# Optimization experiments

Measured on AMD Instinct MI355X. Metric: run time of the kernel, lower is better.

The kernel has to match this reference:

```python
import jax, jax.numpy as jnp
import numpy as np

N_NODES = 100000
N_EDGES = 3200000
DIM = 128
HID = 32


def gcn_conv(x, src, dst, W, b, n):
    # PyG GCNConv: linear transform, add self-loops, symmetric deg normalization,
    # scatter-sum to destination, then bias.
    x = x @ W  # [N, out]
    loops = jnp.arange(n)
    s = jnp.concatenate([src, loops])
    d = jnp.concatenate([dst, loops])
    deg = jax.ops.segment_sum(jnp.ones(s.shape[0], x.dtype), d, num_segments=n)
    dinv = jax.lax.rsqrt(deg)  # deg >= 1 thanks to self-loops
    norm = dinv[s] * dinv[d]   # [E+N]
    out = jax.ops.segment_sum(x[s] * norm[:, None], d, num_segments=n)
    return out + b


def setup_inputs() -> dict:
    key = jax.random.key(0)
    k = jax.random.split(key, 4)
    x = jax.random.normal(k[0], (N_NODES, DIM), dtype=jnp.float32)
    edge_index = jax.random.randint(k[1], (2, N_EDGES), 0, N_NODES)
    W1 = jax.random.normal(k[2], (DIM, HID), dtype=jnp.float32) * (1.0 / np.sqrt(DIM))
    b1 = jnp.zeros((HID,), jnp.float32)
    W2 = jax.random.normal(k[3], (HID, 1), dtype=jnp.float32) * (1.0 / np.sqrt(HID))
    b2 = jnp.zeros((1,), jnp.float32)
    return {"x": x, "edge_index": edge_index, "W1": W1, "b1": b1, "W2": W2, "b2": b2}


def reference(x, edge_index, W1, b1, W2, b2):
    src, dst = edge_index[0], edge_index[1]
    n = x.shape[0]
    h = jax.nn.relu(gcn_conv(x, src, dst, W1, b1, n))        # [N, 32]
    scores = gcn_conv(h, src, dst, W2, b2, n).squeeze(-1)     # [N]
    return (h, scores)
```

## Files before the change

### kernel.cpp

```cpp
#include <hip/hip_runtime.h>
#include <hip/hip_bf16.h>

#define N_NODES 100000
#define N_EDGES 3200000
#define DIM 128
#define HID 32

#define BSH 6
#define BNODES (1 << BSH)
#define NBUK ((N_NODES + BNODES - 1) >> BSH)
#define NBP 2048
#define FCHUNK 8192
#define NFILL ((N_EDGES + FCHUNK - 1) / FCHUNK)
#define CAP 3072

typedef short v8s __attribute__((ext_vector_type(8)));
typedef float v4f __attribute__((ext_vector_type(4)));

__device__ __forceinline__ float bf_lo(unsigned int u) { return __uint_as_float(u << 16); }
__device__ __forceinline__ float bf_hi(unsigned int u) { return __uint_as_float(u & 0xFFFF0000u); }
__device__ __forceinline__ unsigned int pk2(float a, float b) {
    __hip_bfloat162 p = __float22bfloat162_rn(make_float2(a, b));
    union { __hip_bfloat162 h; unsigned int u; } cv; cv.h = p; return cv.u;
}


__global__ void k_zeroB(int* __restrict__ bcnt) {
    int i = blockIdx.x * blockDim.x + threadIdx.x;
    if (i < NBP) bcnt[i] = 0;
}

__launch_bounds__(512)
__global__ void k_bfill(const int* __restrict__ src, const int* __restrict__ dst,
                        int* __restrict__ bcnt, unsigned int* __restrict__ ebuf) {
    __shared__ int cntA[NBP];
    __shared__ int offA[NBP];
    __shared__ int baseG[NBP];
    __shared__ int ssum[512];
    __shared__ unsigned int stage[FCHUNK];
    __shared__ unsigned short sbuk[FCHUNK];
    int t = threadIdx.x;
    int e0 = blockIdx.x * FCHUNK;
    int eN = min(e0 + FCHUNK, N_EDGES) - e0;
    int n4 = eN >> 2;
    const int4* d4 = (const int4*)(dst + e0);
    const int4* s4 = (const int4*)(src + e0);
    int4 dd[4], ss[4];
    #pragma unroll
    for (int k = 0; k < 4; ++k) {
        int i = t + k * 512;
        if (i < n4) { dd[k] = d4[i]; ss[k] = s4[i]; }
    }
    for (int i = t; i < NBP; i += 512) cntA[i] = 0;
    __syncthreads();
    unsigned short rk[16];
    #pragma unroll
    for (int k = 0; k < 4; ++k) {
        int i = t + k * 512;
        if (i < n4) {
            rk[4 * k + 0] = (unsigned short)atomicAdd(&cntA[dd[k].x >> BSH], 1);
            rk[4 * k + 1] = (unsigned short)atomicAdd(&cntA[dd[k].y >> BSH], 1);
            rk[4 * k + 2] = (unsigned short)atomicAdd(&cntA[dd[k].z >> BSH], 1);
            rk[4 * k + 3] = (unsigned short)atomicAdd(&cntA[dd[k].w >> BSH], 1);
        }
    }
    __syncthreads();
    {
        int c[4]; int sum = 0;
        #pragma unroll
        for (int k = 0; k < 4; ++k) { c[k] = cntA[t * 4 + k]; sum += c[k]; }
        ssum[t] = sum; __syncthreads();
        for (int d = 1; d < 512; d <<= 1) {
            int add = (t >= d) ? ssum[t - d] : 0;
            __syncthreads();
            ssum[t] += add;
            __syncthreads();
        }
        int excl = ssum[t] - sum;
        #pragma unroll
        for (int k = 0; k < 4; ++k) { offA[t * 4 + k] = excl; excl += c[k]; }
    }
    __syncthreads();
    for (int b = t; b < NBP; b += 512)
        if (cntA[b] > 0) baseG[b] = b * CAP + atomicAdd(&bcnt[b], cntA[b]);
    #pragma unroll
    for (int k = 0; k < 4; ++k) {
        int i = t + k * 512;
        if (i < n4) {
            int b0 = dd[k].x >> BSH, b1 = dd[k].y >> BSH;
            int b2 = dd[k].z >> BSH, b3 = dd[k].w >> BSH;
            int p0 = offA[b0] + rk[4 * k + 0];
            int p1 = offA[b1] + rk[4 * k + 1];
            int p2 = offA[b2] + rk[4 * k + 2];
            int p3 = offA[b3] + rk[4 * k + 3];
            stage[p0] = ((unsigned int)(dd[k].x & (BNODES - 1)) << 20) | (unsigned int)ss[k].x;
            stage[p1] = ((unsigned int)(dd[k].y & (BNODES - 1)) << 20) | (unsigned int)ss[k].y;
            stage[p2] = ((unsigned int)(dd[k].z & (BNODES - 1)) << 20) | (unsigned int)ss[k].z;
            stage[p3] = ((unsigned int)(dd[k].w & (BNODES - 1)) << 20) | (unsigned int)ss[k].w;
            sbuk[p0] = (unsigned short)b0;
            sbuk[p1] = (unsigned short)b1;
            sbuk[p2] = (unsigned short)b2;
            sbuk[p3] = (unsigned short)b3;
        }
    }
    __syncthreads();
    for (int i = t; i < eN; i += 512) {
        int b = sbuk[i];
        ebuf[baseG[b] + (i - offA[b])] = stage[i];
    }
}

__launch_bounds__(256)
__global__ void k_sort(unsigned int* __restrict__ ebuf, const int* __restrict__ bcnt,
                       int* __restrict__ rowbeg, int* __restrict__ rowend,
                       float* __restrict__ dinv) {
    __shared__ unsigned int slab[CAP];
    __shared__ unsigned int slab2[CAP];
    __shared__ int hist[BNODES];
    __shared__ int scanx[BNODES];
    __shared__ int cur[BNODES];
    int t = threadIdx.x;
    int b = blockIdx.x;
    int s0 = b * CAP;
    int n = min(bcnt[b], CAP);
    if (t < BNODES) hist[t] = 0;
    __syncthreads();
    for (int i = t; i < n; i += 256) {
        unsigned int w = ebuf[s0 + i];
        slab[i] = w;
        atomicAdd(&hist[w >> 20], 1);
    }
    __syncthreads();
    if (t == 0) {
        int r = 0;
        for (int l = 0; l < BNODES; ++l) { scanx[l] = r; r += hist[l]; }
    }
    __syncthreads();
    if (t < BNODES) {
        cur[t] = scanx[t];
        int v = b * BNODES + t;
        if (v < N_NODES) {
            rowbeg[v] = s0 + scanx[t];
            rowend[v] = s0 + scanx[t] + hist[t];
            dinv[v] = rsqrtf((float)(hist[t] + 1));
        }
    }
    __syncthreads();
    for (int i = t; i < n; i += 256) {
        unsigned int w = slab[i];
        int pos = atomicAdd(&cur[w >> 20], 1);
        slab2[pos] = w;
    }
    __syncthreads();
    for (int i = t; i < n; i += 256) ebuf[s0 + i] = slab2[i];
}

__launch_bounds__(256)
__global__ void k_gemm1(const float* __restrict__ x, const float* __restrict__ W1,
                        const float* __restrict__ dinv, unsigned int* __restrict__ y1a,
                        unsigned int* __restrict__ y1b) {
    int wv = (blockIdx.x * 256 + threadIdx.x) >> 6;
    int nwaves = (gridDim.x * 256) >> 6;
    int lane = threadIdx.x & 63;
    int m = lane & 15;
    int kb = lane >> 4;
    v8s Bf[2][4];
    #pragma unroll
    for (int tt = 0; tt < 2; ++tt)
        #pragma unroll
        for (int s = 0; s < 4; ++s) {
            union { unsigned int u[4]; v8s v; } ub;
            #pragma unroll
            for (int jj = 0; jj < 4; ++jj) {
                int k = s * 32 + kb * 8 + jj * 2;
                ub.u[jj] = pk2(W1[k * HID + tt * 16 + m], W1[(k + 1) * HID + tt * 16 + m]);
            }
            Bf[tt][s] = ub.v;
        }
    for (int tile = wv; tile < N_NODES / 16; tile += nwaves) {
        int base = tile * 16;
        const float* xr = x + (size_t)(base + m) * DIM;
        v4f acc0 = {0.f, 0.f, 0.f, 0.f}, acc1 = {0.f, 0.f, 0.f, 0.f};
        #pragma unroll
        for (int s = 0; s < 4; ++s) {
            float4 xa = *(const float4*)(xr + s * 32 + kb * 8);
            float4 xb = *(const float4*)(xr + s * 32 + kb * 8 + 4);
            union { unsigned int u[4]; v8s v; } ua;
            ua.u[0] = pk2(xa.x, xa.y); ua.u[1] = pk2(xa.z, xa.w);
            ua.u[2] = pk2(xb.x, xb.y); ua.u[3] = pk2(xb.z, xb.w);
            acc0 = __builtin_amdgcn_mfma_f32_16x16x32_bf16(ua.v, Bf[0][s], acc0, 0, 0, 0);
            acc1 = __builtin_amdgcn_mfma_f32_16x16x32_bf16(ua.v, Bf[1][s], acc1, 0, 0, 0);
        }
        float4 dv = *(const float4*)(dinv + base + kb * 4);
        float d[4] = {dv.x, dv.y, dv.z, dv.w};
        #pragma unroll
        for (int r = 0; r < 4; ++r) {
            float v0 = acc0[r] * d[r];
            float v1 = acc1[r] * d[r];
            float p0 = __shfl_xor(v0, 1, 64);
            float p1 = __shfl_xor(v1, 1, 64);
            if ((m & 1) == 0) {
                int node = base + kb * 4 + r;
                y1a[node * 8 + (m >> 1)] = pk2(v0, p0);
                y1b[node * 8 + (m >> 1)] = pk2(v1, p1);
            }
        }
    }
}

template <int HALF>
__launch_bounds__(256)
__global__ void k_gather1(const int* __restrict__ rowbeg, const int* __restrict__ rowend,
                          const unsigned int* __restrict__ ebuf,
                          const unsigned int* __restrict__ yh, const float* __restrict__ dinv,
                          const float* __restrict__ b1, const float* __restrict__ W2,
                          float* __restrict__ out_h, float* __restrict__ pA,
                          float* __restrict__ y2) {
    int t = threadIdx.x;
    int node = blockIdx.x * 8 + (t >> 5);
    if (node >= N_NODES) return;
    int lane = t & 31;
    int sub = lane >> 2;
    int c2 = lane & 3;
    int start = rowbeg[node], end = rowend[node];
    float a0[4] = {0.f, 0.f, 0.f, 0.f};
    float a1[4] = {0.f, 0.f, 0.f, 0.f};
    float a2[4] = {0.f, 0.f, 0.f, 0.f};
    float a3[4] = {0.f, 0.f, 0.f, 0.f};
    const uint2* y2b = (const uint2*)yh;
    int j = start;
    for (; j + 32 <= end; j += 32) {
        unsigned int w = ebuf[j + lane];
        unsigned int e0 = (unsigned int)__shfl((int)w, 0  + sub, 32) & 0xFFFFF;
        unsigned int e1 = (unsigned int)__shfl((int)w, 8  + sub, 32) & 0xFFFFF;
        unsigned int e2 = (unsigned int)__shfl((int)w, 16 + sub, 32) & 0xFFFFF;
        unsigned int e3 = (unsigned int)__shfl((int)w, 24 + sub, 32) & 0xFFFFF;
        uint2 v0 = y2b[e0 * 4 + c2];
        uint2 v1 = y2b[e1 * 4 + c2];
        uint2 v2 = y2b[e2 * 4 + c2];
        uint2 v3 = y2b[e3 * 4 + c2];
        a0[0] += bf_lo(v0.x); a0[1] += bf_hi(v0.x); a0[2] += bf_lo(v0.y); a0[3] += bf_hi(v0.y);
        a1[0] += bf_lo(v1.x); a1[1] += bf_hi(v1.x); a1[2] += bf_lo(v1.y); a1[3] += bf_hi(v1.y);
        a2[0] += bf_lo(v2.x); a2[1] += bf_hi(v2.x); a2[2] += bf_lo(v2.y); a2[3] += bf_hi(v2.y);
        a3[0] += bf_lo(v3.x); a3[1] += bf_hi(v3.x); a3[2] += bf_lo(v3.y); a3[3] += bf_hi(v3.y);
    }
    int navail = end - j;
    if (navail > 0) {
        unsigned int w = ebuf[min(j + lane, end - 1)];
        #pragma unroll
        for (int k = 0; k < 4; ++k) {
            int idx = k * 8 + sub;
            unsigned int u = (unsigned int)__shfl((int)w, idx, 32) & 0xFFFFF;
            if (idx < navail) {
                uint2 v = y2b[u * 4 + c2];
                a0[0] += bf_lo(v.x); a0[1] += bf_hi(v.x);
                a0[2] += bf_lo(v.y); a0[3] += bf_hi(v.y);
            }
        }
    }
    float q[4];
    #pragma unroll
    for (int i = 0; i < 4; ++i) q[i] = (a0[i] + a1[i]) + (a2[i] + a3[i]);
    #pragma unroll
    for (int i = 0; i < 4; ++i) {
        q[i] += __shfl_xor(q[i], 4, 32);
        q[i] += __shfl_xor(q[i], 8, 32);
        q[i] += __shfl_xor(q[i], 16, 32);
    }
    uint2 sv = y2b[(unsigned int)node * 4 + c2];
    q[0] += bf_lo(sv.x); q[1] += bf_hi(sv.x); q[2] += bf_lo(sv.y); q[3] += bf_hi(sv.y);
    float di = dinv[node];
    int col = HALF * 16 + 4 * c2;
    float h[4], p = 0.f;
    #pragma unroll
    for (int i = 0; i < 4; ++i) {
        h[i] = fmaxf(fmaf(di, q[i], b1[col + i]), 0.f);
        p = fmaf(h[i], W2[col + i], p);
    }
    p += __shfl_xor(p, 1, 32);
    p += __shfl_xor(p, 2, 32);
    if (sub == 0) {
        *(float4*)&out_h[(size_t)node * HID + col] = make_float4(h[0], h[1], h[2], h[3]);
        if (c2 == 0) {
            if (HALF == 0) pA[node] = p;
            else           y2[node] = di * (pA[node] + p);
        }
    }
}

__launch_bounds__(256)
__global__ void k_gather2(const int* __restrict__ rowbeg, const int* __restrict__ rowend,
                          const unsigned int* __restrict__ ebuf, const float* __restrict__ y2,
                          const float* __restrict__ dinv, const float* __restrict__ b2,
                          float* __restrict__ scores) {
    int t = threadIdx.x;
    int node = blockIdx.x * 8 + (t >> 5);
    int lane = t & 31;
    if (node >= N_NODES) return;
    int start = rowbeg[node], end = rowend[node];
    float acc = 0.f;
    for (int j = start + lane; j < end; j += 32)
        acc += y2[ebuf[j] & 0xFFFFF];
    #pragma unroll
    for (int off = 16; off > 0; off >>= 1) acc += __shfl_xor(acc, off);
    if (lane == 0) scores[node] = dinv[node] * (acc + y2[node]) + b2[0];
}

extern "C" void kernel_launch(void* const* d_in, const int* in_sizes, int n_in,
                              void* d_out, int out_size, void* d_ws, size_t ws_size,
                              hipStream_t stream) {
    const float* x  = (const float*)d_in[0];
    const int* ei   = (const int*)d_in[1];
    const float* W1 = (const float*)d_in[2];
    const float* b1 = (const float*)d_in[3];
    const float* W2 = (const float*)d_in[4];
    const float* b2 = (const float*)d_in[5];

    const int* src = ei;
    const int* dst = ei + N_EDGES;

    int* bcnt = (int*)d_ws;
    unsigned int* ebuf = (unsigned int*)(bcnt + NBP);
    int* rowbeg = (int*)(ebuf + (size_t)NBUK * CAP);
    int* rowend = rowbeg + N_NODES;
    float* dinv = (float*)(rowend + N_NODES);
    unsigned int* y1a = (unsigned int*)(dinv + N_NODES);
    unsigned int* y1b = y1a + (size_t)N_NODES * 8;
    float* pA   = (float*)(y1b + (size_t)N_NODES * 8);
    float* y2   = pA + N_NODES;

    float* out_h = (float*)d_out;
    float* out_s = out_h + (size_t)N_NODES * HID;

    k_zeroB <<<NBP / 256, 256, 0, stream>>>(bcnt);
    k_bfill <<<NFILL, 512, 0, stream>>>(src, dst, bcnt, ebuf);
    k_sort  <<<NBUK, 256, 0, stream>>>(ebuf, bcnt, rowbeg, rowend, dinv);
    k_gemm1 <<<512, 256, 0, stream>>>(x, W1, dinv, y1a, y1b);
    k_gather1<0><<<(N_NODES + 7) / 8, 256, 0, stream>>>(rowbeg, rowend, ebuf, y1a, dinv, b1, W2, out_h, pA, y2);
    k_gather1<1><<<(N_NODES + 7) / 8, 256, 0, stream>>>(rowbeg, rowend, ebuf, y1b, dinv, b1, W2, out_h, pA, y2);
    k_gather2<<<(N_NODES + 7) / 8, 256, 0, stream>>>(rowbeg, rowend, ebuf, y2, dinv, b2, out_s);
}
```

Baseline: 137.1 us.

## Shrink fill chunk, fold bucket offsets, and split sort histogram into sub-counters

Reduces the edge-fill chunk per block from 8192 to 6144 edges, which lowers shared memory per block and raises the block count. It replaces the separate global-base and offset lookups with one precomputed difference array per bucket. In the per-bucket sort kernel, the 64-entry histogram and cursor arrays become four sub-counters per node chosen by thread index, which spreads LDS atomic contention. The cost is extra scan work and more fill blocks issuing global atomics.

After: 146.3 us. 6.7% more time.

```diff
diff --git a/kernel.cpp b/kernel.cpp
--- a/kernel.cpp
+++ b/kernel.cpp
@@ -10,7 +10,7 @@
 #define BNODES (1 << BSH)
 #define NBUK ((N_NODES + BNODES - 1) >> BSH)
 #define NBP 2048
-#define FCHUNK 8192
+#define FCHUNK 6144
 #define NFILL ((N_EDGES + FCHUNK - 1) / FCHUNK)
 #define CAP 3072
 
@@ -35,7 +35,7 @@
                         int* __restrict__ bcnt, unsigned int* __restrict__ ebuf) {
     __shared__ int cntA[NBP];
     __shared__ int offA[NBP];
-    __shared__ int baseG[NBP];
+    __shared__ int diff[NBP];
     __shared__ int ssum[512];
     __shared__ unsigned int stage[FCHUNK];
     __shared__ unsigned short sbuk[FCHUNK];
@@ -45,17 +45,17 @@
     int n4 = eN >> 2;
     const int4* d4 = (const int4*)(dst + e0);
     const int4* s4 = (const int4*)(src + e0);
-    int4 dd[4], ss[4];
-    #pragma unroll
-    for (int k = 0; k < 4; ++k) {
+    int4 dd[3], ss[3];
+    #pragma unroll
+    for (int k = 0; k < 3; ++k) {
         int i = t + k * 512;
         if (i < n4) { dd[k] = d4[i]; ss[k] = s4[i]; }
     }
     for (int i = t; i < NBP; i += 512) cntA[i] = 0;
     __syncthreads();
-    unsigned short rk[16];
-    #pragma unroll
-    for (int k = 0; k < 4; ++k) {
+    unsigned short rk[12];
+    #pragma unroll
+    for (int k = 0; k < 3; ++k) {
         int i = t + k * 512;
         if (i < n4) {
             rk[4 * k + 0] = (unsigned short)atomicAdd(&cntA[dd[k].x >> BSH], 1);
@@ -82,9 +82,9 @@
     }
     __syncthreads();
     for (int b = t; b < NBP; b += 512)
-        if (cntA[b] > 0) baseG[b] = b * CAP + atomicAdd(&bcnt[b], cntA[b]);
-    #pragma unroll
-    for (int k = 0; k < 4; ++k) {
+        if (cntA[b] > 0) diff[b] = b * CAP + atomicAdd(&bcnt[b], cntA[b]) - offA[b];
+    #pragma unroll
+    for (int k = 0; k < 3; ++k) {
         int i = t + k * 512;
         if (i < n4) {
             int b0 = dd[k].x >> BSH, b1 = dd[k].y >> BSH;
@@ -104,10 +104,8 @@
         }
     }
     __syncthreads();
-    for (int i = t; i < eN; i += 512) {
-        int b = sbuk[i];
-        ebuf[baseG[b] + (i - offA[b])] = stage[i];
-    }
+    for (int i = t; i < eN; i += 512)
+        ebuf[diff[sbuk[i]] + i] = stage[i];
 }
 
 __launch_bounds__(256)
@@ -116,39 +114,50 @@
                        float* __restrict__ dinv) {
     __shared__ unsigned int slab[CAP];
     __shared__ unsigned int slab2[CAP];
-    __shared__ int hist[BNODES];
+    __shared__ int hist4[BNODES * 4];
     __shared__ int scanx[BNODES];
-    __shared__ int cur[BNODES];
+    __shared__ int cur4[BNODES * 4];
     int t = threadIdx.x;
     int b = blockIdx.x;
     int s0 = b * CAP;
     int n = min(bcnt[b], CAP);
-    if (t < BNODES) hist[t] = 0;
-    __syncthreads();
+    if (t < BNODES * 4) hist4[t] = 0;
+    __syncthreads();
+    int sub = t & 3;
     for (int i = t; i < n; i += 256) {
         unsigned int w = ebuf[s0 + i];
         slab[i] = w;
-        atomicAdd(&hist[w >> 20], 1);
+        atomicAdd(&hist4[((w >> 20) << 2) + sub], 1);
     }
     __syncthreads();
     if (t == 0) {
         int r = 0;
-        for (int l = 0; l < BNODES; ++l) { scanx[l] = r; r += hist[l]; }
+        for (int l = 0; l < BNODES; ++l) {
+            scanx[l] = r;
+            r += hist4[l * 4] + hist4[l * 4 + 1] + hist4[l * 4 + 2] + hist4[l * 4 + 3];
+        }
     }
     __syncthreads();
     if (t < BNODES) {
-        cur[t] = scanx[t];
+        int h0 = hist4[t * 4], h1 = hist4[t * 4 + 1];
+        int h2 = hist4[t * 4 + 2], h3 = hist4[t * 4 + 3];
+        int base = scanx[t];
+        cur4[t * 4 + 0] = base;
+        cur4[t * 4 + 1] = base + h0;
+        cur4[t * 4 + 2] = base + h0 + h1;
+        cur4[t * 4 + 3] = base + h0 + h1 + h2;
+        int deg = h0 + h1 + h2 + h3;
         int v = b * BNODES + t;
         if (v < N_NODES) {
-            rowbeg[v] = s0 + scanx[t];
-            rowend[v] = s0 + scanx[t] + hist[t];
-            dinv[v] = rsqrtf((float)(hist[t] + 1));
+            rowbeg[v] = s0 + base;
+            rowend[v] = s0 + base + deg;
+            dinv[v] = rsqrtf((float)(deg + 1));
         }
     }
     __syncthreads();
     for (int i = t; i < n; i += 256) {
         unsigned int w = slab[i];
-        int pos = atomicAdd(&cur[w >> 20], 1);
+        int pos = atomicAdd(&cur4[((w >> 20) << 2) + sub], 1);
         slab2[pos] = w;
     }
     __syncthreads();
```
